# Performance work log

Measured on AMD Instinct MI355X. Metric: run time of the kernel, lower is better.

Reference implementation:

```python
import jax, jax.numpy as jnp
import numpy as np

T, B, I = 2048, 256, 64
H = 1280          # hidden_size = 20 * input_size
H4 = H // 4       # fc2 out / LSTMCell input = 320
H8 = H // 8       # LSTMCell hidden = 160
O = 32            # output_size


def setup_inputs() -> dict:
    key = jax.random.key(0)
    ks = jax.random.split(key, 12)
    n = lambda k, shape, fan: jax.random.normal(k, shape, jnp.float32) * (1.0 / np.sqrt(fan))
    return {
        "inputs": jax.random.normal(ks[0], (T, B, I), jnp.float32),
        "W1": n(ks[1], (H, I), I),
        "b1": jnp.zeros((H,), jnp.float32),
        "W2": n(ks[2], (H4, H), H),
        "b2": jnp.zeros((H4,), jnp.float32),
        "W_ih": n(ks[3], (4 * H8, H4), H4),
        "W_hh": n(ks[4], (4 * H8, H8), H8),
        "b_ih": jnp.zeros((4 * H8,), jnp.float32),
        "b_hh": jnp.zeros((4 * H8,), jnp.float32),
        "W3": n(ks[5], (O, H8), H8),
        "b3": jnp.zeros((O,), jnp.float32),
    }


def reference(inputs, W1, b1, W2, b2, W_ih, W_hh, b_ih, b_hh, W3, b3):
    # Eval-mode forward: dropout / noise are identity when not training.
    Bd = inputs.shape[1]
    Hc = W_hh.shape[1]

    def step(carry, x_t):
        h, c = carry
        x = jax.nn.leaky_relu(x_t @ W1.T + b1)          # [B, H]
        x = jax.nn.leaky_relu(x @ W2.T + b2)            # [B, H//4]
        gates = x @ W_ih.T + b_ih + h @ W_hh.T + b_hh   # [B, 4*H//8]
        i, f, g, o = jnp.split(gates, 4, axis=-1)       # PyTorch gate order i,f,g,o
        i = jax.nn.sigmoid(i)
        f = jax.nn.sigmoid(f)
        g = jnp.tanh(g)
        o = jax.nn.sigmoid(o)
        c = f * c + i * g
        h = o * jnp.tanh(c)
        y = h @ W3.T + b3                                # [B, O]
        return (h, c), y

    h0 = jnp.zeros((Bd, Hc), inputs.dtype)
    c0 = jnp.zeros((Bd, Hc), inputs.dtype)
    _, ys = jax.lax.scan(step, (h0, c0), inputs)         # [T, B, O]
    return ys
```

## Files before the change

### kernel.cpp

```cpp
#include <hip/hip_runtime.h>
#include <hip/hip_bf16.h>

#define T_STEPS 2048
#define BATCH   256
#define INW     64
#define H1      1280
#define H4D     320
#define H8D     160
#define G4      640
#define ONUM    32

typedef __attribute__((ext_vector_type(8))) short short8;
typedef __attribute__((ext_vector_type(4))) float floatx4;
typedef __hip_bfloat16 bf16;

union frag8 { short8 v; uint2 u2[2]; };

__device__ __forceinline__ float b2f(bf16 v) { return __bfloat162float(v); }
__device__ __forceinline__ bf16  f2b(float v) { return __float2bfloat16(v); }
__device__ __forceinline__ float bfu(unsigned short u) { return __uint_as_float((unsigned)u << 16); }
__device__ __forceinline__ float fsig(float x)  { return __fdividef(1.0f, 1.0f + __expf(-x)); }
__device__ __forceinline__ float ftanh(float x) { return __fdividef(2.0f, 1.0f + __expf(-2.0f * x)) - 1.0f; }

__device__ __forceinline__ void lds_barrier() {
  asm volatile("s_waitcnt lgkmcnt(0)\n\ts_barrier" ::: "memory");
}

struct bf16x4 { bf16 a, b, c, d; };
__global__ void cast_f32_bf16_v4(const float* __restrict__ s, bf16* __restrict__ d, int n4) {
  int i = blockIdx.x * blockDim.x + threadIdx.x;
  if (i >= n4) return;
  float4 v = reinterpret_cast<const float4*>(s)[i];
  bf16x4 o{f2b(v.x), f2b(v.y), f2b(v.z), f2b(v.w)};
  reinterpret_cast<bf16x4*>(d)[i] = o;
}

__global__ void cast_permute_wih(const float* __restrict__ s, bf16* __restrict__ d) {
  int i = blockIdx.x * blockDim.x + threadIdx.x;
  if (i >= G4 * (H4D / 4)) return;
  int p = i / (H4D / 4), k4 = (i - p * (H4D / 4)) * 4;
  int g = p & 3, ix = p >> 2;
  float4 v = *reinterpret_cast<const float4*>(&s[(size_t)(g * 160 + ix) * H4D + k4]);
  bf16x4 o{f2b(v.x), f2b(v.y), f2b(v.z), f2b(v.w)};
  *reinterpret_cast<bf16x4*>(&d[(size_t)p * H4D + k4]) = o;
}

#define SMEM_BYTES 65024

__device__ void fused_gemm(char* smem, int tid, int gb,
    const bf16* __restrict__ Xg, const bf16* __restrict__ W1g, const float* __restrict__ b1v,
    const bf16* __restrict__ W2g, const float* __restrict__ b2v,
    const bf16* __restrict__ Wpg, const float* __restrict__ bihv, const float* __restrict__ bhhv,
    bf16* __restrict__ gxw)
{
  bf16 (*Y1s)[72]  = reinterpret_cast<bf16 (*)[72]>(smem);
  bf16 (*W2cs)[72] = reinterpret_cast<bf16 (*)[72]>(smem + 9216);
  const int lane = tid & 63, wave = tid >> 6;
  const int mrow = lane & 15, quad = lane >> 4;
  const int wm = (wave >= 5) ? 1 : 0;
  const int wn = wave - wm * 5;
  const int fm = wave & 3;
  const int fnp = (wave >> 2) & 1;
  const size_t R0 = (size_t)gb * 64;

  short8 xf0, xf1;
  if (wave < 8) {
    const bf16* xrow = Xg + (R0 + fm * 16 + mrow) * INW;
    xf0 = *reinterpret_cast<const short8*>(xrow + quad * 8);
    xf1 = *reinterpret_cast<const short8*>(xrow + 32 + quad * 8);
  }

  short8 w1f[4];
  if (wave < 8) {
    const bf16* wr0 = W1g + (size_t)((fnp * 2 + 0) * 16 + mrow) * INW;
    const bf16* wr1 = W1g + (size_t)((fnp * 2 + 1) * 16 + mrow) * INW;
    w1f[0] = *reinterpret_cast<const short8*>(wr0 + quad * 8);
    w1f[1] = *reinterpret_cast<const short8*>(wr0 + 32 + quad * 8);
    w1f[2] = *reinterpret_cast<const short8*>(wr1 + quad * 8);
    w1f[3] = *reinterpret_cast<const short8*>(wr1 + 32 + quad * 8);
  }

  short8 w2r[4];
#pragma unroll
  for (int i = 0; i < 4; ++i) {
    int v = tid + i * 640;
    w2r[i] = *reinterpret_cast<const short8*>(&W2g[(size_t)(v >> 3) * H1 + (v & 7) * 8]);
  }
#pragma unroll
  for (int i = 0; i < 4; ++i) {
    int v = tid + i * 640;
    *reinterpret_cast<short8*>(&W2cs[v >> 3][(v & 7) * 8]) = w2r[i];
  }

  floatx4 acc2[2][4] = {};

  for (int c = 0; c < 20; ++c) {
    if (wave < 8) {
      floatx4 a10 = {}, a11 = {};
      a10 = __builtin_amdgcn_mfma_f32_16x16x32_bf16(xf0, w1f[0], a10, 0, 0, 0);
      a10 = __builtin_amdgcn_mfma_f32_16x16x32_bf16(xf1, w1f[1], a10, 0, 0, 0);
      a11 = __builtin_amdgcn_mfma_f32_16x16x32_bf16(xf0, w1f[2], a11, 0, 0, 0);
      a11 = __builtin_amdgcn_mfma_f32_16x16x32_bf16(xf1, w1f[3], a11, 0, 0, 0);
      if (c < 19) {
        const bf16* wr0 = W1g + (size_t)((c + 1) * 64 + (fnp * 2 + 0) * 16 + mrow) * INW;
        const bf16* wr1 = W1g + (size_t)((c + 1) * 64 + (fnp * 2 + 1) * 16 + mrow) * INW;
        w1f[0] = *reinterpret_cast<const short8*>(wr0 + quad * 8);
        w1f[1] = *reinterpret_cast<const short8*>(wr0 + 32 + quad * 8);
        w1f[2] = *reinterpret_cast<const short8*>(wr1 + quad * 8);
        w1f[3] = *reinterpret_cast<const short8*>(wr1 + 32 + quad * 8);
      }
#pragma unroll
      for (int r = 0; r < 4; ++r) {
        int row = fm * 16 + quad * 4 + r;
        {
          int col = (fnp * 2 + 0) * 16 + mrow;
          float vv = a10[r] + b1v[c * 64 + col];
          Y1s[row][col] = f2b(vv > 0.0f ? vv : 0.01f * vv);
        }
        {
          int col = (fnp * 2 + 1) * 16 + mrow;
          float vv = a11[r] + b1v[c * 64 + col];
          Y1s[row][col] = f2b(vv > 0.0f ? vv : 0.01f * vv);
        }
      }
    }
    if (c < 19) {
#pragma unroll
      for (int i = 0; i < 4; ++i) {
        int v = tid + i * 640;
        w2r[i] = *reinterpret_cast<const short8*>(
            &W2g[(size_t)(v >> 3) * H1 + (c + 1) * 64 + (v & 7) * 8]);
      }
    }
    lds_barrier();
#pragma unroll
    for (int kk = 0; kk < 2; ++kk) {
      short8 af0 = *reinterpret_cast<const short8*>(&Y1s[wm * 32 + mrow][kk * 32 + quad * 8]);
      short8 af1 = *reinterpret_cast<const short8*>(&Y1s[wm * 32 + 16 + mrow][kk * 32 + quad * 8]);
#pragma unroll
      for (int j = 0; j < 4; ++j) {
        short8 bfj = *reinterpret_cast<const short8*>(
            &W2cs[wn * 64 + j * 16 + mrow][kk * 32 + quad * 8]);
        acc2[0][j] = __builtin_amdgcn_mfma_f32_16x16x32_bf16(af0, bfj, acc2[0][j], 0, 0, 0);
        acc2[1][j] = __builtin_amdgcn_mfma_f32_16x16x32_bf16(af1, bfj, acc2[1][j], 0, 0, 0);
      }
    }
    lds_barrier();
    if (c < 19) {
#pragma unroll
      for (int i = 0; i < 4; ++i) {
        int v = tid + i * 640;
        *reinterpret_cast<short8*>(&W2cs[v >> 3][(v & 7) * 8]) = w2r[i];
      }
    }
  }

  bf16 (*Y2s)[328] = reinterpret_cast<bf16 (*)[328]>(smem);
  char* Wps = smem + 41984;
  short8 wpr[2];
#pragma unroll
  for (int i = 0; i < 2; ++i) {
    int v = tid + i * 640;
    wpr[i] = *reinterpret_cast<const short8*>(&Wpg[(size_t)(v >> 2) * H4D + (v & 3) * 8]);
  }
#pragma unroll
  for (int i = 0; i < 2; ++i) {
#pragma unroll
    for (int j = 0; j < 4; ++j) {
      int col = wn * 64 + j * 16 + mrow;
      float bb = b2v[col];
#pragma unroll
      for (int r = 0; r < 4; ++r) {
        int row = wm * 32 + i * 16 + quad * 4 + r;
        float vv = acc2[i][j][r] + bb;
        Y2s[row][col] = f2b(vv > 0.0f ? vv : 0.01f * vv);
      }
    }
  }
#pragma unroll
  for (int i = 0; i < 2; ++i) {
    int v = tid + i * 640;
    frag8 u; u.v = wpr[i];
    char* p = Wps + (size_t)(v >> 2) * 72 + (v & 3) * 16;
    *reinterpret_cast<uint2*>(p) = u.u2[0];
    *reinterpret_cast<uint2*>(p + 8) = u.u2[1];
  }
  lds_barrier();

  floatx4 ag[2][4];
  for (int t = 0; t < 20; ++t) {
    int h = t / 10, kc = t - h * 10;
    if (kc == 0) {
#pragma unroll
      for (int i = 0; i < 2; ++i)
#pragma unroll
        for (int j = 0; j < 4; ++j) ag[i][j] = (floatx4){0.f, 0.f, 0.f, 0.f};
    }
    short8 af0 = *reinterpret_cast<const short8*>(&Y2s[wm * 32 + mrow][kc * 32 + quad * 8]);
    short8 af1 = *reinterpret_cast<const short8*>(&Y2s[wm * 32 + 16 + mrow][kc * 32 + quad * 8]);
    frag8 bfj[4];
#pragma unroll
    for (int j = 0; j < 4; ++j) {
      const char* p = Wps + (size_t)(wn * 64 + j * 16 + mrow) * 72 + quad * 16;
      bfj[j].u2[0] = *reinterpret_cast<const uint2*>(p);
      bfj[j].u2[1] = *reinterpret_cast<const uint2*>(p + 8);
    }
#pragma unroll
    for (int j = 0; j < 4; ++j) {
      ag[0][j] = __builtin_amdgcn_mfma_f32_16x16x32_bf16(af0, bfj[j].v, ag[0][j], 0, 0, 0);
      ag[1][j] = __builtin_amdgcn_mfma_f32_16x16x32_bf16(af1, bfj[j].v, ag[1][j], 0, 0, 0);
    }
    if (t < 19) {
      int nh = (t + 1) / 10, nk = (t + 1) - nh * 10;
#pragma unroll
      for (int i = 0; i < 2; ++i) {
        int v = tid + i * 640;
        wpr[i] = *reinterpret_cast<const short8*>(
            &Wpg[(size_t)(nh * 320 + (v >> 2)) * H4D + nk * 32 + (v & 3) * 8]);
      }
    }
    lds_barrier();
    if (t < 19) {
#pragma unroll
      for (int i = 0; i < 2; ++i) {
        int v = tid + i * 640;
        frag8 u; u.v = wpr[i];
        char* p = Wps + (size_t)(v >> 2) * 72 + (v & 3) * 16;
        *reinterpret_cast<uint2*>(p) = u.u2[0];
        *reinterpret_cast<uint2*>(p + 8) = u.u2[1];
      }
    }
    lds_barrier();
    if (kc == 9) {
#pragma unroll
      for (int j = 0; j < 4; ++j) {
        int p = h * 320 + wn * 64 + j * 16 + mrow;
        int g = p & 3, ix = p >> 2;
        float bb = bihv[g * 160 + ix] + bhhv[g * 160 + ix];
#pragma unroll
        for (int i = 0; i < 2; ++i)
#pragma unroll
          for (int r = 0; r < 4; ++r) {
            int row = wm * 32 + i * 16 + quad * 4 + r;
            gxw[(R0 + row) * 640 + p] = f2b(ag[i][j][r] + bb);
          }
      }
    }
  }
}

__device__ void recur_path(char* smem, int tid, int bid,
    const bf16* __restrict__ gx, const bf16* __restrict__ Whh,
    const bf16* __restrict__ W3w, const float* __restrict__ b3,
    bf16* __restrict__ h_ws, float* __restrict__ c_ws,
    float* __restrict__ outp, int Tc, int init)
{
  bf16 (*hbuf)[16][168] = reinterpret_cast<bf16 (*)[16][168]>(smem);
  bf16 (*w3s)[168] = reinterpret_cast<bf16 (*)[168]>(smem + 10752);
  const int lane = tid & 63;
  const int wave = tid >> 6;
  const int mrow = lane & 15;
  const int quad = lane >> 4;
  const int bbase = bid * 4;
  const int ixg = wave * 16 + mrow;

  short8 whf[4][5];
#pragma unroll
  for (int g = 0; g < 4; ++g)
#pragma unroll
    for (int ks = 0; ks < 5; ++ks)
      whf[g][ks] = *reinterpret_cast<const short8*>(
          &Whh[(size_t)(g * 160 + ixg) * 160 + ks * 32 + quad * 8]);

  for (int e = tid; e < 32 * 160; e += 640) {
    int r = e / 160, cix = e - r * 160;
    w3s[r][cix] = W3w[e];
  }
  const float b3v = (wave < 2) ? b3[wave * 16 + mrow] : 0.0f;

  for (int e = tid; e < 2 * 16 * 168; e += 640)
    reinterpret_cast<bf16*>(hbuf)[e] = f2b(0.0f);
  __syncthreads();
  {
    int r = tid / 160, cix = tid - r * 160;
    hbuf[0][r * 4][cix] = init ? f2b(0.0f) : h_ws[(size_t)(bbase + r) * 160 + cix];
  }
  float c0 = init ? 0.0f : c_ws[(size_t)(bbase + quad) * 160 + ixg];
  __syncthreads();

  const uint2* __restrict__ gxp = reinterpret_cast<const uint2*>(gx);
  const size_t goff = (size_t)(bbase + quad) * 160 + ixg;
  uint2 gcur = gxp[goff], gnext = gcur;

  for (int t = 0; t < Tc; ++t) {
    const int rb = t & 1, wb = rb ^ 1;
    if (t + 1 < Tc) gnext = gxp[(size_t)(t + 1) * (256 * 160) + goff];

    short8 af[5];
#pragma unroll
    for (int ks = 0; ks < 5; ++ks)
      af[ks] = *reinterpret_cast<const short8*>(&hbuf[rb][mrow][ks * 32 + quad * 8]);

    if (wave < 2 && t > 0) {
      short8 w3f[5];
#pragma unroll
      for (int ks = 0; ks < 5; ++ks)
        w3f[ks] = *reinterpret_cast<const short8*>(&w3s[wave * 16 + mrow][ks * 32 + quad * 8]);
      floatx4 ya = {};
#pragma unroll
      for (int ks = 0; ks < 5; ++ks)
        ya = __builtin_amdgcn_mfma_f32_16x16x32_bf16(af[ks], w3f[ks], ya, 0, 0, 0);
      outp[((size_t)(t - 1) * 256 + bbase + quad) * 32 + wave * 16 + mrow] = ya[0] + b3v;
    }

    floatx4 acc[4] = {};
#pragma unroll
    for (int ks = 0; ks < 5; ++ks)
#pragma unroll
      for (int g = 0; g < 4; ++g)
        acc[g] = __builtin_amdgcn_mfma_f32_16x16x32_bf16(af[ks], whf[g][ks], acc[g], 0, 0, 0);

    {
      union { uint2 u; unsigned short s[4]; } q;
      q.u = gcur;
      float xi = acc[0][0] + bfu(q.s[0]);
      float xf = acc[1][0] + bfu(q.s[1]);
      float xg = acc[2][0] + bfu(q.s[2]);
      float xo = acc[3][0] + bfu(q.s[3]);
      float iv = fsig(xi), fv = fsig(xf), gvv = ftanh(xg), ov = fsig(xo);
      c0 = fv * c0 + iv * gvv;
      hbuf[wb][quad * 4][ixg] = f2b(ov * ftanh(c0));
    }
    gcur = gnext;
    lds_barrier();
  }

  if (wave < 2) {
    const int rb = Tc & 1;
    short8 af[5], w3f[5];
#pragma unroll
    for (int ks = 0; ks < 5; ++ks) {
      af[ks]  = *reinterpret_cast<const short8*>(&hbuf[rb][mrow][ks * 32 + quad * 8]);
      w3f[ks] = *reinterpret_cast<const short8*>(&w3s[wave * 16 + mrow][ks * 32 + quad * 8]);
    }
    floatx4 ya = {};
#pragma unroll
    for (int ks = 0; ks < 5; ++ks)
      ya = __builtin_amdgcn_mfma_f32_16x16x32_bf16(af[ks], w3f[ks], ya, 0, 0, 0);
    outp[((size_t)(Tc - 1) * 256 + bbase + quad) * 32 + wave * 16 + mrow] = ya[0] + b3v;
  }

  {
    int r = tid / 160, cix = tid - r * 160;
    h_ws[(size_t)(bbase + r) * 160 + cix] = hbuf[Tc & 1][r * 4][cix];
  }
  c_ws[(size_t)(bbase + quad) * 160 + ixg] = c0;
}

__global__ __launch_bounds__(640, 1) void fused_step(
    int has_recur, const bf16* gxr, const bf16* Whh, const bf16* W3w,
    const float* b3, bf16* h_ws, float* c_ws, float* outp, int Tc, int init,
    int has_gemm, const bf16* Xc, const bf16* W1w, const float* b1v,
    const bf16* W2w, const float* b2v, const bf16* Wpw,
    const float* bihv, const float* bhhv, bf16* gxw)
{
  __shared__ __align__(16) char smem[SMEM_BYTES];
  const int tid = threadIdx.x;
  if (blockIdx.x < 64) {
    if (has_recur)
      recur_path(smem, tid, blockIdx.x, gxr, Whh, W3w, b3, h_ws, c_ws, outp, Tc, init);
    return;
  }
  if (has_gemm)
    fused_gemm(smem, tid, blockIdx.x - 64, Xc, W1w, b1v, W2w, b2v, Wpw, bihv, bhhv, gxw);
}

extern "C" void kernel_launch(void* const* d_in, const int* in_sizes, int n_in,
                              void* d_out, int out_size, void* d_ws, size_t ws_size,
                              hipStream_t stream)
{
  const float* inp = (const float*)d_in[0];
  const float* W1  = (const float*)d_in[1];
  const float* b1  = (const float*)d_in[2];
  const float* W2  = (const float*)d_in[3];
  const float* b2  = (const float*)d_in[4];
  const float* Wih = (const float*)d_in[5];
  const float* Whh = (const float*)d_in[6];
  const float* bih = (const float*)d_in[7];
  const float* bhh = (const float*)d_in[8];
  const float* W3  = (const float*)d_in[9];
  const float* b3  = (const float*)d_in[10];
  float* out = (float*)d_out;

  char* ws = (char*)d_ws;
  size_t off = 0;
  auto alloc = [&](size_t bytes) -> char* {
    char* p = ws + off;
    off += (bytes + 255) & ~(size_t)255;
    return p;
  };

  bf16* inpb = (bf16*)alloc((size_t)T_STEPS * BATCH * INW * 2);
  bf16* w1b  = (bf16*)alloc((size_t)H1 * INW * 2);
  bf16* w2b  = (bf16*)alloc((size_t)H4D * H1 * 2);
  bf16* wpb  = (bf16*)alloc((size_t)G4 * H4D * 2);
  bf16* whhb = (bf16*)alloc((size_t)G4 * H8D * 2);
  bf16* w3b  = (bf16*)alloc((size_t)ONUM * H8D * 2);
  bf16* h_ws = (bf16*)alloc((size_t)BATCH * H8D * 2);
  float* c_ws = (float*)alloc((size_t)BATCH * H8D * 4);
  size_t fixed = off;

  int Tc = 128;
  while (Tc > 16) {
    size_t Mc = (size_t)Tc * BATCH;
    size_t need = fixed + 2 * ((Mc * G4 * 2 + 255) & ~(size_t)255);
    if (need <= ws_size) break;
    Tc >>= 1;
  }
  const size_t Mc = (size_t)Tc * BATCH;
  bf16* gxb[2];
  for (int i = 0; i < 2; ++i) gxb[i] = (bf16*)alloc(Mc * G4 * 2);

  {
    int n4 = T_STEPS * BATCH * INW / 4;
    cast_f32_bf16_v4<<<(n4 + 255) / 256, 256, 0, stream>>>(inp, inpb, n4);
    n4 = H1 * INW / 4;
    cast_f32_bf16_v4<<<(n4 + 255) / 256, 256, 0, stream>>>(W1, w1b, n4);
    n4 = H4D * H1 / 4;
    cast_f32_bf16_v4<<<(n4 + 255) / 256, 256, 0, stream>>>(W2, w2b, n4);
    int np = G4 * (H4D / 4);
    cast_permute_wih<<<(np + 255) / 256, 256, 0, stream>>>(Wih, wpb);
    n4 = G4 * H8D / 4;
    cast_f32_bf16_v4<<<(n4 + 255) / 256, 256, 0, stream>>>(Whh, whhb, n4);
    n4 = ONUM * H8D / 4;
    cast_f32_bf16_v4<<<(n4 + 255) / 256, 256, 0, stream>>>(W3, w3b, n4);
  }

  const int nch = T_STEPS / Tc;
  const int nGB = (int)(Mc / 64);

  for (int L = 0; L <= nch; ++L) {
    const int hg = (L < nch) ? 1 : 0;
    const int hr = (L >= 1) ? 1 : 0;
    const bf16* Xc = inpb + (size_t)(hg ? L : 0) * Mc * INW;
    bf16* gxw = gxb[L & 1];
    const bf16* gxr = gxb[(L + 1) & 1];
    float* outp = hr ? (out + (size_t)(L - 1) * Tc * BATCH * ONUM) : out;

    fused_step<<<64 + (hg ? nGB : 0), 640, 0, stream>>>(
        hr, gxr, whhb, w3b, b3, h_ws, c_ws, outp, Tc, (L == 1) ? 1 : 0,
        hg, Xc, w1b, b1, w2b, b2, wpb, bih, bhh, gxw);
  }
}
```

Before: 2.779 ms.

## Move output projection off the recurrence path into a pipelined batched GEMM stage

The recurrent blocks no longer compute y = h·W3ᵀ+b3 inside the sequential time loop. They write each h_t to a chunk buffer instead. A new ygemm block type computes the output projection for a chunk one launch later, so it overlaps with the next chunk's recurrence and input GEMM, and the pipeline gains one extra stage. The time loop is also unrolled by two so the double-buffer indices are static. The cost is extra global-memory traffic for the h history and added workspace.

```diff
diff --git a/kernel.cpp b/kernel.cpp
--- a/kernel.cpp
+++ b/kernel.cpp
@@ -251,12 +251,10 @@
 
 __device__ void recur_path(char* smem, int tid, int bid,
     const bf16* __restrict__ gx, const bf16* __restrict__ Whh,
-    const bf16* __restrict__ W3w, const float* __restrict__ b3,
     bf16* __restrict__ h_ws, float* __restrict__ c_ws,
-    float* __restrict__ outp, int Tc, int init)
+    bf16* __restrict__ hh, int Tc, int init)
 {
   bf16 (*hbuf)[16][168] = reinterpret_cast<bf16 (*)[16][168]>(smem);
-  bf16 (*w3s)[168] = reinterpret_cast<bf16 (*)[168]>(smem + 10752);
   const int lane = tid & 63;
   const int wave = tid >> 6;
   const int mrow = lane & 15;
@@ -272,12 +270,6 @@
       whf[g][ks] = *reinterpret_cast<const short8*>(
           &Whh[(size_t)(g * 160 + ixg) * 160 + ks * 32 + quad * 8]);
 
-  for (int e = tid; e < 32 * 160; e += 640) {
-    int r = e / 160, cix = e - r * 160;
-    w3s[r][cix] = W3w[e];
-  }
-  const float b3v = (wave < 2) ? b3[wave * 16 + mrow] : 0.0f;
-
   for (int e = tid; e < 2 * 16 * 168; e += 640)
     reinterpret_cast<bf16*>(hbuf)[e] = f2b(0.0f);
   __syncthreads();
@@ -290,89 +282,101 @@
 
   const uint2* __restrict__ gxp = reinterpret_cast<const uint2*>(gx);
   const size_t goff = (size_t)(bbase + quad) * 160 + ixg;
-  uint2 gcur = gxp[goff], gnext = gcur;
-
-  for (int t = 0; t < Tc; ++t) {
-    const int rb = t & 1, wb = rb ^ 1;
-    if (t + 1 < Tc) gnext = gxp[(size_t)(t + 1) * (256 * 160) + goff];
-
+
+  auto body = [&](int t, int rb, uint2 g) {
     short8 af[5];
 #pragma unroll
     for (int ks = 0; ks < 5; ++ks)
       af[ks] = *reinterpret_cast<const short8*>(&hbuf[rb][mrow][ks * 32 + quad * 8]);
-
-    if (wave < 2 && t > 0) {
-      short8 w3f[5];
-#pragma unroll
-      for (int ks = 0; ks < 5; ++ks)
-        w3f[ks] = *reinterpret_cast<const short8*>(&w3s[wave * 16 + mrow][ks * 32 + quad * 8]);
-      floatx4 ya = {};
-#pragma unroll
-      for (int ks = 0; ks < 5; ++ks)
-        ya = __builtin_amdgcn_mfma_f32_16x16x32_bf16(af[ks], w3f[ks], ya, 0, 0, 0);
-      outp[((size_t)(t - 1) * 256 + bbase + quad) * 32 + wave * 16 + mrow] = ya[0] + b3v;
-    }
-
     floatx4 acc[4] = {};
 #pragma unroll
     for (int ks = 0; ks < 5; ++ks)
 #pragma unroll
-      for (int g = 0; g < 4; ++g)
-        acc[g] = __builtin_amdgcn_mfma_f32_16x16x32_bf16(af[ks], whf[g][ks], acc[g], 0, 0, 0);
-
-    {
-      union { uint2 u; unsigned short s[4]; } q;
-      q.u = gcur;
-      float xi = acc[0][0] + bfu(q.s[0]);
-      float xf = acc[1][0] + bfu(q.s[1]);
-      float xg = acc[2][0] + bfu(q.s[2]);
-      float xo = acc[3][0] + bfu(q.s[3]);
-      float iv = fsig(xi), fv = fsig(xf), gvv = ftanh(xg), ov = fsig(xo);
-      c0 = fv * c0 + iv * gvv;
-      hbuf[wb][quad * 4][ixg] = f2b(ov * ftanh(c0));
-    }
-    gcur = gnext;
-    lds_barrier();
-  }
-
-  if (wave < 2) {
-    const int rb = Tc & 1;
-    short8 af[5], w3f[5];
-#pragma unroll
-    for (int ks = 0; ks < 5; ++ks) {
-      af[ks]  = *reinterpret_cast<const short8*>(&hbuf[rb][mrow][ks * 32 + quad * 8]);
-      w3f[ks] = *reinterpret_cast<const short8*>(&w3s[wave * 16 + mrow][ks * 32 + quad * 8]);
-    }
-    floatx4 ya = {};
-#pragma unroll
-    for (int ks = 0; ks < 5; ++ks)
-      ya = __builtin_amdgcn_mfma_f32_16x16x32_bf16(af[ks], w3f[ks], ya, 0, 0, 0);
-    outp[((size_t)(Tc - 1) * 256 + bbase + quad) * 32 + wave * 16 + mrow] = ya[0] + b3v;
+      for (int g4 = 0; g4 < 4; ++g4)
+        acc[g4] = __builtin_amdgcn_mfma_f32_16x16x32_bf16(af[ks], whf[g4][ks], acc[g4], 0, 0, 0);
+    union { uint2 u; unsigned short s[4]; } q;
+    q.u = g;
+    float xi = acc[0][0] + bfu(q.s[0]);
+    float xf = acc[1][0] + bfu(q.s[1]);
+    float xg = acc[2][0] + bfu(q.s[2]);
+    float xo = acc[3][0] + bfu(q.s[3]);
+    float iv = fsig(xi), fv = fsig(xf), gvv = ftanh(xg), ov = fsig(xo);
+    c0 = fv * c0 + iv * gvv;
+    bf16 hv = f2b(ov * ftanh(c0));
+    hbuf[rb ^ 1][quad * 4][ixg] = hv;
+    hh[((size_t)t * 256 + bbase + quad) * 160 + ixg] = hv;
+  };
+
+  uint2 g0 = gxp[goff];
+  uint2 g1 = gxp[(size_t)(256 * 160) + goff];
+  for (int t = 0; t < Tc; t += 2) {
+    body(t, 0, g0);
+    if (t + 2 < Tc) g0 = gxp[(size_t)(t + 2) * (256 * 160) + goff];
+    lds_barrier();
+    body(t + 1, 1, g1);
+    if (t + 3 < Tc) g1 = gxp[(size_t)(t + 3) * (256 * 160) + goff];
+    lds_barrier();
   }
 
   {
     int r = tid / 160, cix = tid - r * 160;
-    h_ws[(size_t)(bbase + r) * 160 + cix] = hbuf[Tc & 1][r * 4][cix];
+    h_ws[(size_t)(bbase + r) * 160 + cix] = hbuf[0][r * 4][cix];
   }
   c_ws[(size_t)(bbase + quad) * 160 + ixg] = c0;
 }
 
+__device__ void ygemm(int tid, int yb, const bf16* __restrict__ hh,
+                      const bf16* __restrict__ W3w, const float* __restrict__ b3,
+                      float* __restrict__ outy)
+{
+  const int lane = tid & 63, wave = tid >> 6;
+  if (wave >= 8) return;
+  const int mrow = lane & 15, quad = lane >> 4;
+  const size_t R0 = (size_t)yb * 128 + wave * 16;
+  short8 af[5], bf0[5], bf1[5];
+#pragma unroll
+  for (int ks = 0; ks < 5; ++ks) {
+    af[ks]  = *reinterpret_cast<const short8*>(&hh[(R0 + mrow) * 160 + ks * 32 + quad * 8]);
+    bf0[ks] = *reinterpret_cast<const short8*>(&W3w[(size_t)mrow * 160 + ks * 32 + quad * 8]);
+    bf1[ks] = *reinterpret_cast<const short8*>(&W3w[(size_t)(16 + mrow) * 160 + ks * 32 + quad * 8]);
+  }
+  floatx4 a0 = {}, a1 = {};
+#pragma unroll
+  for (int ks = 0; ks < 5; ++ks) {
+    a0 = __builtin_amdgcn_mfma_f32_16x16x32_bf16(af[ks], bf0[ks], a0, 0, 0, 0);
+    a1 = __builtin_amdgcn_mfma_f32_16x16x32_bf16(af[ks], bf1[ks], a1, 0, 0, 0);
+  }
+  float bb0 = b3[mrow], bb1 = b3[16 + mrow];
+#pragma unroll
+  for (int r = 0; r < 4; ++r) {
+    size_t row = R0 + quad * 4 + r;
+    outy[row * 32 + mrow] = a0[r] + bb0;
+    outy[row * 32 + 16 + mrow] = a1[r] + bb1;
+  }
+}
+
 __global__ __launch_bounds__(640, 1) void fused_step(
-    int has_recur, const bf16* gxr, const bf16* Whh, const bf16* W3w,
-    const float* b3, bf16* h_ws, float* c_ws, float* outp, int Tc, int init,
-    int has_gemm, const bf16* Xc, const bf16* W1w, const float* b1v,
+    int has_recur, const bf16* gxr, const bf16* Whh,
+    bf16* h_ws, float* c_ws, bf16* hh_w, int Tc, int init,
+    int nbg, const bf16* Xc, const bf16* W1w, const float* b1v,
     const bf16* W2w, const float* b2v, const bf16* Wpw,
-    const float* bihv, const float* bhhv, bf16* gxw)
+    const float* bihv, const float* bhhv, bf16* gxw,
+    int has_y, const bf16* hh_r, const bf16* W3w, const float* b3, float* outy)
 {
   __shared__ __align__(16) char smem[SMEM_BYTES];
   const int tid = threadIdx.x;
   if (blockIdx.x < 64) {
     if (has_recur)
-      recur_path(smem, tid, blockIdx.x, gxr, Whh, W3w, b3, h_ws, c_ws, outp, Tc, init);
+      recur_path(smem, tid, blockIdx.x, gxr, Whh, h_ws, c_ws, hh_w, Tc, init);
     return;
   }
-  if (has_gemm)
-    fused_gemm(smem, tid, blockIdx.x - 64, Xc, W1w, b1v, W2w, b2v, Wpw, bihv, bhhv, gxw);
+  int gb = blockIdx.x - 64;
+  if (gb < nbg) {
+    fused_gemm(smem, tid, gb, Xc, W1w, b1v, W2w, b2v, Wpw, bihv, bhhv, gxw);
+    return;
+  }
+  if (has_y)
+    ygemm(tid, gb - nbg, hh_r, W3w, b3, outy);
 }
 
 extern "C" void kernel_launch(void* const* d_in, const int* in_sizes, int n_in,
@@ -413,13 +417,16 @@
   int Tc = 128;
   while (Tc > 16) {
     size_t Mc = (size_t)Tc * BATCH;
-    size_t need = fixed + 2 * ((Mc * G4 * 2 + 255) & ~(size_t)255);
+    size_t need = fixed
+      + 2 * ((Mc * G4 * 2 + 255) & ~(size_t)255)
+      + 2 * ((Mc * H8D * 2 + 255) & ~(size_t)255);
     if (need <= ws_size) break;
     Tc >>= 1;
   }
   const size_t Mc = (size_t)Tc * BATCH;
-  bf16* gxb[2];
+  bf16* gxb[2], *hhb[2];
   for (int i = 0; i < 2; ++i) gxb[i] = (bf16*)alloc(Mc * G4 * 2);
+  for (int i = 0; i < 2; ++i) hhb[i] = (bf16*)alloc(Mc * H8D * 2);
 
   {
     int n4 = T_STEPS * BATCH * INW / 4;
@@ -438,17 +445,26 @@
 
   const int nch = T_STEPS / Tc;
   const int nGB = (int)(Mc / 64);
-
-  for (int L = 0; L <= nch; ++L) {
+  const int nYB = (int)(Mc / 128);
+
+  for (int L = 0; L <= nch + 1; ++L) {
     const int hg = (L < nch) ? 1 : 0;
-    const int hr = (L >= 1) ? 1 : 0;
-    const bf16* Xc = inpb + (size_t)(hg ? L : 0) * Mc * INW;
-    bf16* gxw = gxb[L & 1];
-    const bf16* gxr = gxb[(L + 1) & 1];
-    float* outp = hr ? (out + (size_t)(L - 1) * Tc * BATCH * ONUM) : out;
-
-    fused_step<<<64 + (hg ? nGB : 0), 640, 0, stream>>>(
-        hr, gxr, whhb, w3b, b3, h_ws, c_ws, outp, Tc, (L == 1) ? 1 : 0,
-        hg, Xc, w1b, b1, w2b, b2, wpb, bih, bhh, gxw);
-  }
-}
+    const int hr = (L >= 1 && L <= nch) ? 1 : 0;
+    const int hy = (L >= 2) ? 1 : 0;
+    const int cg = L, cr = L - 1, cy = L - 2;
+
+    const bf16* Xc = inpb + (size_t)(hg ? cg : 0) * Mc * INW;
+    bf16* gxw = gxb[cg & 1];
+    const bf16* gxr = gxb[(hr ? cr : 0) & 1];
+    bf16* hh_w = hhb[(hr ? cr : 0) & 1];
+    const bf16* hh_r = hhb[(hy ? cy : 0) & 1];
+    float* outy = out + (size_t)(hy ? cy : 0) * Tc * BATCH * ONUM;
+    const int nbg = hg ? nGB : 0;
+    const int nby = hy ? nYB : 0;
+
+    fused_step<<<64 + nbg + nby, 640, 0, stream>>>(
+        hr, gxr, whhb, h_ws, c_ws, hh_w, Tc, (cr == 0) ? 1 : 0,
+        nbg, Xc, w1b, b1, w2b, b2, wpb, bih, bhh, gxw,
+        hy, hh_r, w3b, b3, outy);
+  }
+}
```

Result: no change. 2.764 ms (-0.6%).
